# Kernel optimization log

Hardware: AMD Instinct MI355X
Metric: run time of the kernel (lower is better)

Reference implementation:

```python
import jax, jax.numpy as jnp
import numpy as np

B, T, E = 2048, 200, 64
H1, H2 = 64, 16
EPS = 1e-8


def dice(x, alpha):
    # Dice activation: standardize over (batch, seq) per feature, then
    # p = sigmoid(x_norm); out = p*x + (1-p)*alpha*x
    mean = jnp.mean(x, axis=(0, 1), keepdims=True)
    var = jnp.var(x, axis=(0, 1), keepdims=True)
    x_norm = (x - mean) * jax.lax.rsqrt(var + EPS)
    p = jax.nn.sigmoid(x_norm)
    return p * x + (1.0 - p) * alpha * x


def setup_inputs() -> dict:
    key = jax.random.key(0)
    ks = jax.random.split(key, 9)
    d_in = 4 * E
    return {
        "query_ad": jax.random.normal(ks[0], (B, 1, E), jnp.float32),
        "hist_behavior": jax.random.normal(ks[1], (B, T, E), jnp.float32),
        "hist_behavior_length": jax.random.randint(ks[2], (B,), 0, T, jnp.int64 if jax.config.jax_enable_x64 else jnp.int32),
        "W1": jax.random.normal(ks[3], (d_in, H1), jnp.float32) / np.sqrt(d_in),
        "b1": jnp.zeros((H1,), jnp.float32),
        "alpha1": jnp.zeros((H1,), jnp.float32),
        "W2": jax.random.normal(ks[4], (H1, H2), jnp.float32) / np.sqrt(H1),
        "b2": jnp.zeros((H2,), jnp.float32),
        "alpha2": jnp.zeros((H2,), jnp.float32),
    }


def reference(query_ad, hist_behavior, hist_behavior_length, W1, b1, alpha1, W2, b2, alpha2):
    Tlen = hist_behavior.shape[1]
    q = jnp.broadcast_to(query_ad, hist_behavior.shape)          # [B,T,E]
    att_in = jnp.concatenate(
        [q, hist_behavior, q - hist_behavior, q * hist_behavior], axis=-1
    )                                                            # [B,T,4E]
    h = dice(att_in @ W1 + b1, alpha1)                           # [B,T,H1]
    logits = dice(h @ W2 + b2, alpha2)                           # [B,T,H2]
    logits = jnp.swapaxes(logits, 1, 2)                          # [B,H2,T]
    mask = jnp.arange(Tlen)[None, :] < hist_behavior_length[:, None]  # [B,T]
    masked = jnp.where(mask[:, None, :], jnp.float32(1e-9), logits)
    score = jax.nn.softmax(masked, axis=-1)                      # [B,H2,T]
    out = jnp.einsum('bht,bte->bhe', score, hist_behavior)       # [B,H2,E]
    return out
```

## Files before the change

kernel.cpp:

```cpp
#include <hip/hip_runtime.h>
#include <math.h>


typedef float f4 __attribute__((ext_vector_type(4)));
typedef float f32x4 __attribute__((ext_vector_type(4)));
typedef short s8v __attribute__((ext_vector_type(8)));
typedef short s4v __attribute__((ext_vector_type(4)));
typedef unsigned short u16;

#define B_   2048
#define T_   200
#define BT_  409600
#define NB1  3200
#define NB2  1600

static __device__ __forceinline__ u16 f2bf(float f) {
  union { float f; unsigned u; } v; v.f = f;
  unsigned r = v.u + 0x7fffu + ((v.u >> 16) & 1u);
  return (u16)(r >> 16);
}
static __device__ __forceinline__ float bf2f(u16 s) {
  union { unsigned u; float f; } v; v.u = ((unsigned)s) << 16;
  return v.f;
}

__global__ __launch_bounds__(256) void k_qw(
    const float* __restrict__ q, const float* __restrict__ W1,
    const float* __restrict__ b1, float* __restrict__ qW) {
  __shared__ float Wac[64 * 65];
  __shared__ float ql[16 * 64];
  const int tid = threadIdx.x;
#pragma unroll
  for (int i = 0; i < 16; i++) {
    int idx = tid + 256 * i;
    int k = idx >> 6, j = idx & 63;
    Wac[k * 65 + j] = W1[k * 64 + j] + W1[(128 + k) * 64 + j];
  }
  const int b0 = blockIdx.x * 16;
#pragma unroll
  for (int i = 0; i < 4; i++) {
    int idx = tid + 256 * i;
    ql[idx] = q[(size_t)b0 * 64 + idx];
  }
  __syncthreads();
  const int wv = tid >> 6, lane = tid & 63;
#pragma unroll
  for (int ii = 0; ii < 4; ii++) {
    const int bl = wv * 4 + ii;
    float acc = b1[lane];
#pragma unroll 8
    for (int k = 0; k < 64; k++) acc += ql[bl * 64 + k] * Wac[k * 65 + lane];
    qW[(size_t)(b0 + bl) * 64 + lane] = acc;
  }
}

__global__ __launch_bounds__(256) void k_wprep(
    const float* __restrict__ W1, u16* __restrict__ wsWT) {
  int t = threadIdx.x + blockIdx.x * 256;
  int n = t >> 7, k = t & 127;
  float w = (k < 64) ? (W1[(64 + k) * 64 + n] - W1[(128 + k) * 64 + n])
                     : W1[(128 + k) * 64 + n];
  wsWT[t] = f2bf(w);
}

__global__ __launch_bounds__(256, 3) void k_gemm1(
    const float* __restrict__ q, const float* __restrict__ hist,
    const u16* __restrict__ wsWT, const float* __restrict__ qW,
    u16* __restrict__ z1, float* __restrict__ part1) {
  __shared__ __align__(16) u16 As[128 * 136];
  __shared__ __align__(16) u16 Ws[64 * 136];
  const int tid = threadIdx.x;
  const int R0 = blockIdx.x * 128;

#pragma unroll
  for (int i = 0; i < 4; i++) {
    int piece = tid + 256 * i;
    int n = piece >> 4, k8 = piece & 15;
    *(s8v*)(Ws + n * 136 + 8 * k8) = *(const s8v*)(wsWT + n * 128 + 8 * k8);
  }
#pragma unroll
  for (int i = 0; i < 8; i++) {
    int piece = tid + 256 * i;
    int row = piece >> 4, c4 = piece & 15;
    int R = R0 + row;
    int b = (int)((unsigned)R / 200u);
    f4 h4 = *(const f4*)(hist + (size_t)R * 64 + 4 * c4);
    f4 q4 = *(const f4*)(q + (size_t)b * 64 + 4 * c4);
    f4 p4 = h4 * q4;
    s4v hv, pv;
#pragma unroll
    for (int j = 0; j < 4; j++) { hv[j] = (short)f2bf(h4[j]); pv[j] = (short)f2bf(p4[j]); }
    *(s4v*)(As + row * 136 + 4 * c4) = hv;
    *(s4v*)(As + row * 136 + 64 + 4 * c4) = pv;
  }
  __syncthreads();

  const int wv = tid >> 6, lane = tid & 63;
  const int lm = lane & 15, quad = lane >> 4;
  f32x4 acc[2][4];
#pragma unroll
  for (int mt = 0; mt < 2; mt++)
#pragma unroll
    for (int nt = 0; nt < 4; nt++) acc[mt][nt] = (f32x4)0.f;

#pragma unroll
  for (int c = 0; c < 4; c++) {
    const int ko = 32 * c + 8 * quad;
    s8v a0 = *(const s8v*)(As + (32 * wv + lm) * 136 + ko);
    s8v a1 = *(const s8v*)(As + (32 * wv + 16 + lm) * 136 + ko);
#pragma unroll
    for (int nt = 0; nt < 4; nt++) {
      s8v b8 = *(const s8v*)(Ws + (16 * nt + lm) * 136 + ko);
      acc[0][nt] = __builtin_amdgcn_mfma_f32_16x16x32_bf16(a0, b8, acc[0][nt], 0, 0, 0);
      acc[1][nt] = __builtin_amdgcn_mfma_f32_16x16x32_bf16(a1, b8, acc[1][nt], 0, 0, 0);
    }
  }
  __syncthreads();

  u16* zs = As;
  float* red = (float*)Ws;
  const int g = wv * 4 + quad;
  float s[4] = {0.f, 0.f, 0.f, 0.f}, sq[4] = {0.f, 0.f, 0.f, 0.f};
#pragma unroll
  for (int mt = 0; mt < 2; mt++)
#pragma unroll
    for (int nt = 0; nt < 4; nt++)
#pragma unroll
      for (int r = 0; r < 4; r++) {
        int row = 32 * wv + 16 * mt + 4 * quad + r;
        int R = R0 + row;
        int b = (int)((unsigned)R / 200u);
        int col = 16 * nt + lm;
        float v = acc[mt][nt][r] + qW[(size_t)b * 64 + col];
        s[nt] += v; sq[nt] += v * v;
        zs[row * 72 + col] = f2bf(v);
      }
#pragma unroll
  for (int nt = 0; nt < 4; nt++) {
    red[g * 64 + 16 * nt + lm] = s[nt];
    red[1024 + g * 64 + 16 * nt + lm] = sq[nt];
  }
  __syncthreads();
#pragma unroll
  for (int i = 0; i < 4; i++) {
    int piece = tid + 256 * i;
    int row = piece >> 3, seg = piece & 7;
    s8v v = *(const s8v*)(zs + row * 72 + 8 * seg);
    *(s8v*)(z1 + (size_t)(R0 + row) * 64 + 8 * seg) = v;
  }
  if (tid < 64) {
    float ss = 0.f, qq = 0.f;
#pragma unroll
    for (int gg = 0; gg < 16; gg++) { ss += red[gg * 64 + tid]; qq += red[1024 + gg * 64 + tid]; }
    part1[(size_t)blockIdx.x * 128 + tid] = ss;
    part1[(size_t)blockIdx.x * 128 + 64 + tid] = qq;
  }
}

__global__ __launch_bounds__(256) void k_finalize(
    const float* __restrict__ part, float* __restrict__ statout,
    int nj, int stride, int nb, float invN) {
  const int j = blockIdx.x, tid = threadIdx.x;
  float s = 0.f, qq = 0.f;
  for (int i = tid; i < nb; i += 256) {
    s += part[(size_t)i * stride + j];
    qq += part[(size_t)i * stride + nj + j];
  }
#pragma unroll
  for (int off = 32; off > 0; off >>= 1) {
    s += __shfl_down(s, off);
    qq += __shfl_down(qq, off);
  }
  __shared__ float rs[4], rq[4];
  if ((tid & 63) == 0) { rs[tid >> 6] = s; rq[tid >> 6] = qq; }
  __syncthreads();
  if (tid == 0) {
    s = rs[0] + rs[1] + rs[2] + rs[3];
    qq = rq[0] + rq[1] + rq[2] + rq[3];
    float mean = s * invN;
    float var = qq * invN - mean * mean;
    statout[j] = mean;
    statout[nj + j] = rsqrtf(var + 1e-8f);
  }
}

__global__ __launch_bounds__(256) void k_gemm2(
    const u16* __restrict__ z1, const float* __restrict__ W2g,
    const float* __restrict__ b2, const float* __restrict__ alpha1,
    const float* __restrict__ stat1, float* __restrict__ z2,
    float* __restrict__ part2) {
  __shared__ float W2l[64 * 16];
  __shared__ float cf[208];
  __shared__ float red[256 * 33];
  const int tid = threadIdx.x;
  if (tid < 64) {
    cf[tid] = stat1[tid];
    cf[64 + tid] = stat1[64 + tid];
    cf[128 + tid] = alpha1[tid];
  }
  if (tid < 16) cf[192 + tid] = b2[tid];
#pragma unroll
  for (int i = 0; i < 4; i++) { int idx = tid + 256 * i; W2l[idx] = W2g[idx]; }
  __syncthreads();
  const size_t row = (size_t)blockIdx.x * 256 + tid;
  const u16* zr = z1 + row * 64;
  float acc[16];
#pragma unroll
  for (int j = 0; j < 16; j++) acc[j] = cf[192 + j];
  for (int k0 = 0; k0 < 64; k0 += 8) {
    s8v x8 = *(const s8v*)(zr + k0);
#pragma unroll
    for (int dk = 0; dk < 8; dk++) {
      int k = k0 + dk;
      float x = bf2f((u16)x8[dk]);
      float xn = (x - cf[k]) * cf[64 + k];
      float p = 1.f / (1.f + __expf(-xn));
      float h = x * (p + (1.f - p) * cf[128 + k]);
#pragma unroll
      for (int jc = 0; jc < 4; jc++) {
        f4 w = *(const f4*)(W2l + k * 16 + 4 * jc);
#pragma unroll
        for (int jj = 0; jj < 4; jj++) acc[4 * jc + jj] += h * w[jj];
      }
    }
  }
#pragma unroll
  for (int jc = 0; jc < 4; jc++) {
    f4 o;
#pragma unroll
    for (int jj = 0; jj < 4; jj++) o[jj] = acc[4 * jc + jj];
    *(f4*)(z2 + row * 16 + 4 * jc) = o;
  }
#pragma unroll
  for (int j = 0; j < 16; j++) {
    red[tid * 33 + j] = acc[j];
    red[tid * 33 + 16 + j] = acc[j] * acc[j];
  }
  __syncthreads();
  if (tid < 32) {
    float s = 0.f;
    for (int g = 0; g < 256; g++) s += red[g * 33 + tid];
    part2[(size_t)blockIdx.x * 32 + tid] = s;
  }
}

__global__ __launch_bounds__(256) void k_attn(
    const float* __restrict__ hist, const float* __restrict__ z2,
    const int* __restrict__ lens, const float* __restrict__ alpha2,
    const float* __restrict__ stat2, float* __restrict__ out) {
  __shared__ float lm[200 * 17];
  __shared__ float sc[16 * 200];
  const int tid = threadIdx.x;
  const int b = blockIdx.x;
  const int L = lens[b];
  {
    const int j = tid & 15, tb = tid >> 4;
    const float mu = stat2[j], rs = stat2[16 + j], al = alpha2[j];
    const float* z2b = z2 + (size_t)b * 3200;
#pragma unroll
    for (int i = 0; i < 13; i++) {
      int t = tb + 16 * i;
      if (t < 200) {
        float x = z2b[t * 16 + j];
        float xn = (x - mu) * rs;
        float p = 1.f / (1.f + __expf(-xn));
        float lg = x * (p + (1.f - p) * al);
        lm[t * 17 + j] = (t < L) ? 1e-9f : lg;
      }
    }
  }
  __syncthreads();
  {
    const int h = tid >> 4, s = tid & 15;
    float v[13];
    float m = -1e30f;
#pragma unroll
    for (int i = 0; i < 13; i++) {
      int t = s + 16 * i;
      float x = (t < 200) ? lm[t * 17 + h] : -1e30f;
      v[i] = x;
      m = fmaxf(m, x);
    }
#pragma unroll
    for (int mk = 8; mk > 0; mk >>= 1) m = fmaxf(m, __shfl_xor(m, mk, 16));
    float sum = 0.f;
#pragma unroll
    for (int i = 0; i < 13; i++) {
      int t = s + 16 * i;
      if (t < 200) { float e = __expf(v[i] - m); v[i] = e; sum += e; }
    }
#pragma unroll
    for (int mk = 8; mk > 0; mk >>= 1) sum += __shfl_xor(sum, mk, 16);
    const float inv = 1.f / sum;
#pragma unroll
    for (int i = 0; i < 13; i++) {
      int t = s + 16 * i;
      if (t < 200) sc[h * 200 + t] = v[i] * inv;
    }
  }
  __syncthreads();
  {
    const int h = tid >> 4, e0 = (tid & 15) * 4;
    const float* hb = hist + (size_t)b * 200 * 64 + e0;
    const float* sh = sc + h * 200;
    f4 acc = 0.f;
    for (int t = 0; t < 200; t += 4) {
      f4 h0 = *(const f4*)(hb + (size_t)t * 64);
      f4 h1 = *(const f4*)(hb + (size_t)(t + 1) * 64);
      f4 h2 = *(const f4*)(hb + (size_t)(t + 2) * 64);
      f4 h3 = *(const f4*)(hb + (size_t)(t + 3) * 64);
      acc += h0 * sh[t];
      acc += h1 * sh[t + 1];
      acc += h2 * sh[t + 2];
      acc += h3 * sh[t + 3];
    }
    *(f4*)(out + (size_t)b * 1024 + tid * 4) = acc;
  }
}

extern "C" void kernel_launch(void* const* d_in, const int* in_sizes, int n_in,
                              void* d_out, int out_size, void* d_ws, size_t ws_size,
                              hipStream_t stream) {
  const float* q    = (const float*)d_in[0];
  const float* hist = (const float*)d_in[1];
  const int*   len  = (const int*)d_in[2];
  const float* W1   = (const float*)d_in[3];
  const float* b1   = (const float*)d_in[4];
  const float* al1  = (const float*)d_in[5];
  const float* W2   = (const float*)d_in[6];
  const float* b2   = (const float*)d_in[7];
  const float* al2  = (const float*)d_in[8];
  float* out = (float*)d_out;

  char* ws = (char*)d_ws;
  u16*   z1    = (u16*)ws;
  float* z2    = (float*)(ws + 52428800);
  float* qW    = (float*)(ws + 52428800 + 26214400);
  u16*   wsWT  = (u16*)((char*)qW + 524288);
  float* part1 = (float*)((char*)wsWT + 16384);
  float* part2 = part1 + (size_t)NB1 * 128;
  float* stat1 = part2 + (size_t)NB2 * 32;
  float* stat2 = stat1 + 128;
  (void)ws_size; (void)in_sizes; (void)n_in; (void)out_size;

  k_qw<<<dim3(128), dim3(256), 0, stream>>>(q, W1, b1, qW);
  k_wprep<<<dim3(32), dim3(256), 0, stream>>>(W1, wsWT);
  k_gemm1<<<dim3(NB1), dim3(256), 0, stream>>>(q, hist, wsWT, qW, z1, part1);
  k_finalize<<<dim3(64), dim3(256), 0, stream>>>(part1, stat1, 64, 128, NB1, 1.f / (float)BT_);
  k_gemm2<<<dim3(NB2), dim3(256), 0, stream>>>(z1, W2, b2, al1, stat1, z2, part2);
  k_finalize<<<dim3(16), dim3(256), 0, stream>>>(part2, stat2, 16, 32, NB2, 1.f / (float)BT_);
  k_attn<<<dim3(B_), dim3(256), 0, stream>>>(hist, z2, len, al2, stat2, out);
}
```

Measured before the change: 282.7 us.

## Use MFMA for attention pooling, store z2 in bf16, fuse weight prep

Result: faster. 255.6 us (-9.6%).

```diff
diff --git a/kernel.cpp b/kernel.cpp
--- a/kernel.cpp
+++ b/kernel.cpp
@@ -26,7 +26,8 @@
 
 __global__ __launch_bounds__(256) void k_qw(
     const float* __restrict__ q, const float* __restrict__ W1,
-    const float* __restrict__ b1, float* __restrict__ qW) {
+    const float* __restrict__ b1, float* __restrict__ qW,
+    u16* __restrict__ wsWT) {
   __shared__ float Wac[64 * 65];
   __shared__ float ql[16 * 64];
   const int tid = threadIdx.x;
@@ -52,15 +53,13 @@
     for (int k = 0; k < 64; k++) acc += ql[bl * 64 + k] * Wac[k * 65 + lane];
     qW[(size_t)(b0 + bl) * 64 + lane] = acc;
   }
-}
-
-__global__ __launch_bounds__(256) void k_wprep(
-    const float* __restrict__ W1, u16* __restrict__ wsWT) {
-  int t = threadIdx.x + blockIdx.x * 256;
-  int n = t >> 7, k = t & 127;
-  float w = (k < 64) ? (W1[(64 + k) * 64 + n] - W1[(128 + k) * 64 + n])
-                     : W1[(128 + k) * 64 + n];
-  wsWT[t] = f2bf(w);
+  if (blockIdx.x < 32) {
+    int t = blockIdx.x * 256 + tid;
+    int n = t >> 7, k = t & 127;
+    float w = (k < 64) ? (W1[(64 + k) * 64 + n] - W1[(128 + k) * 64 + n])
+                       : W1[(128 + k) * 64 + n];
+    wsWT[t] = f2bf(w);
+  }
 }
 
 __global__ __launch_bounds__(256, 3) void k_gemm1(
@@ -96,7 +95,7 @@
   __syncthreads();
 
   const int wv = tid >> 6, lane = tid & 63;
-  const int lm = lane & 15, quad = lane >> 4;
+  const int lm16 = lane & 15, quad = lane >> 4;
   f32x4 acc[2][4];
 #pragma unroll
   for (int mt = 0; mt < 2; mt++)
@@ -106,11 +105,11 @@
 #pragma unroll
   for (int c = 0; c < 4; c++) {
     const int ko = 32 * c + 8 * quad;
-    s8v a0 = *(const s8v*)(As + (32 * wv + lm) * 136 + ko);
-    s8v a1 = *(const s8v*)(As + (32 * wv + 16 + lm) * 136 + ko);
+    s8v a0 = *(const s8v*)(As + (32 * wv + lm16) * 136 + ko);
+    s8v a1 = *(const s8v*)(As + (32 * wv + 16 + lm16) * 136 + ko);
 #pragma unroll
     for (int nt = 0; nt < 4; nt++) {
-      s8v b8 = *(const s8v*)(Ws + (16 * nt + lm) * 136 + ko);
+      s8v b8 = *(const s8v*)(Ws + (16 * nt + lm16) * 136 + ko);
       acc[0][nt] = __builtin_amdgcn_mfma_f32_16x16x32_bf16(a0, b8, acc[0][nt], 0, 0, 0);
       acc[1][nt] = __builtin_amdgcn_mfma_f32_16x16x32_bf16(a1, b8, acc[1][nt], 0, 0, 0);
     }
@@ -130,15 +129,15 @@
         int row = 32 * wv + 16 * mt + 4 * quad + r;
         int R = R0 + row;
         int b = (int)((unsigned)R / 200u);
-        int col = 16 * nt + lm;
+        int col = 16 * nt + lm16;
         float v = acc[mt][nt][r] + qW[(size_t)b * 64 + col];
         s[nt] += v; sq[nt] += v * v;
         zs[row * 72 + col] = f2bf(v);
       }
 #pragma unroll
   for (int nt = 0; nt < 4; nt++) {
-    red[g * 64 + 16 * nt + lm] = s[nt];
-    red[1024 + g * 64 + 16 * nt + lm] = sq[nt];
+    red[g * 64 + 16 * nt + lm16] = s[nt];
+    red[1024 + g * 64 + 16 * nt + lm16] = sq[nt];
   }
   __syncthreads();
 #pragma unroll
@@ -187,7 +186,7 @@
 __global__ __launch_bounds__(256) void k_gemm2(
     const u16* __restrict__ z1, const float* __restrict__ W2g,
     const float* __restrict__ b2, const float* __restrict__ alpha1,
-    const float* __restrict__ stat1, float* __restrict__ z2,
+    const float* __restrict__ stat1, u16* __restrict__ z2,
     float* __restrict__ part2) {
   __shared__ float W2l[64 * 16];
   __shared__ float cf[208];
@@ -224,49 +223,71 @@
       }
     }
   }
-#pragma unroll
-  for (int jc = 0; jc < 4; jc++) {
-    f4 o;
-#pragma unroll
-    for (int jj = 0; jj < 4; jj++) o[jj] = acc[4 * jc + jj];
-    *(f4*)(z2 + row * 16 + 4 * jc) = o;
-  }
+  s8v o0, o1;
+#pragma unroll
+  for (int jj = 0; jj < 8; jj++) { o0[jj] = (short)f2bf(acc[jj]); o1[jj] = (short)f2bf(acc[8 + jj]); }
+  *(s8v*)(z2 + row * 16) = o0;
+  *(s8v*)(z2 + row * 16 + 8) = o1;
 #pragma unroll
   for (int j = 0; j < 16; j++) {
     red[tid * 33 + j] = acc[j];
     red[tid * 33 + 16 + j] = acc[j] * acc[j];
   }
   __syncthreads();
-  if (tid < 32) {
-    float s = 0.f;
-    for (int g = 0; g < 256; g++) s += red[g * 33 + tid];
-    part2[(size_t)blockIdx.x * 32 + tid] = s;
-  }
-}
-
-__global__ __launch_bounds__(256) void k_attn(
-    const float* __restrict__ hist, const float* __restrict__ z2,
+  const int f = tid >> 3, sub = tid & 7;
+  float s = 0.f;
+  for (int g = sub; g < 256; g += 8) s += red[g * 33 + f];
+  s += __shfl_down(s, 4, 8);
+  s += __shfl_down(s, 2, 8);
+  s += __shfl_down(s, 1, 8);
+  if (sub == 0) part2[(size_t)blockIdx.x * 32 + f] = s;
+}
+
+__global__ __launch_bounds__(256, 3) void k_attn(
+    const float* __restrict__ hist, const u16* __restrict__ z2,
     const int* __restrict__ lens, const float* __restrict__ alpha2,
     const float* __restrict__ stat2, float* __restrict__ out) {
   __shared__ float lm[200 * 17];
-  __shared__ float sc[16 * 200];
+  __shared__ __align__(16) u16 scb[16 * 232];
+  __shared__ __align__(16) u16 hT[64 * 232];
+  __shared__ float cf2[48];
   const int tid = threadIdx.x;
   const int b = blockIdx.x;
   const int L = lens[b];
+  if (tid < 16) {
+    cf2[tid] = stat2[tid];
+    cf2[16 + tid] = stat2[16 + tid];
+    cf2[32 + tid] = alpha2[tid];
+  }
+  __syncthreads();
   {
-    const int j = tid & 15, tb = tid >> 4;
-    const float mu = stat2[j], rs = stat2[16 + j], al = alpha2[j];
-    const float* z2b = z2 + (size_t)b * 3200;
-#pragma unroll
-    for (int i = 0; i < 13; i++) {
-      int t = tb + 16 * i;
-      if (t < 200) {
-        float x = z2b[t * 16 + j];
-        float xn = (x - mu) * rs;
-        float p = 1.f / (1.f + __expf(-xn));
-        float lg = x * (p + (1.f - p) * al);
-        lm[t * 17 + j] = (t < L) ? 1e-9f : lg;
-      }
+    s8v zz = {0, 0, 0, 0, 0, 0, 0, 0};
+    for (int p = tid; p < 320; p += 256) {
+      if (p < 64) { int r = p >> 2, c = p & 3; *(s8v*)(scb + r * 232 + 200 + 8 * c) = zz; }
+      else { int pp = p - 64; int r = pp >> 2, c = pp & 3; *(s8v*)(hT + r * 232 + 200 + 8 * c) = zz; }
+    }
+  }
+  const float* hb = hist + (size_t)b * 200 * 64;
+#pragma unroll
+  for (int i = 0; i < 13; i++) {
+    int p = tid + 256 * i;
+    if (p < 3200) {
+      int t = p >> 4, eq = p & 15;
+      f4 h4 = *(const f4*)(hb + t * 64 + 4 * eq);
+#pragma unroll
+      for (int jj = 0; jj < 4; jj++) hT[(4 * eq + jj) * 232 + t] = f2bf(h4[jj]);
+    }
+  }
+  if (tid < 200) {
+    const u16* zr = z2 + ((size_t)b * 200 + tid) * 16;
+    s8v x0 = *(const s8v*)zr, x1 = *(const s8v*)(zr + 8);
+#pragma unroll
+    for (int j = 0; j < 16; j++) {
+      float x = bf2f((u16)(j < 8 ? x0[j] : x1[j - 8]));
+      float xn = (x - cf2[j]) * cf2[16 + j];
+      float p = 1.f / (1.f + __expf(-xn));
+      float lg = x * (p + (1.f - p) * cf2[32 + j]);
+      lm[tid * 17 + j] = (tid < L) ? 1e-9f : lg;
     }
   }
   __syncthreads();
@@ -295,26 +316,26 @@
 #pragma unroll
     for (int i = 0; i < 13; i++) {
       int t = s + 16 * i;
-      if (t < 200) sc[h * 200 + t] = v[i] * inv;
+      if (t < 200) scb[h * 232 + t] = f2bf(v[i] * inv);
     }
   }
   __syncthreads();
   {
-    const int h = tid >> 4, e0 = (tid & 15) * 4;
-    const float* hb = hist + (size_t)b * 200 * 64 + e0;
-    const float* sh = sc + h * 200;
-    f4 acc = 0.f;
-    for (int t = 0; t < 200; t += 4) {
-      f4 h0 = *(const f4*)(hb + (size_t)t * 64);
-      f4 h1 = *(const f4*)(hb + (size_t)(t + 1) * 64);
-      f4 h2 = *(const f4*)(hb + (size_t)(t + 2) * 64);
-      f4 h3 = *(const f4*)(hb + (size_t)(t + 3) * 64);
-      acc += h0 * sh[t];
-      acc += h1 * sh[t + 1];
-      acc += h2 * sh[t + 2];
-      acc += h3 * sh[t + 3];
-    }
-    *(f4*)(out + (size_t)b * 1024 + tid * 4) = acc;
+    const int wv = tid >> 6, lane = tid & 63;
+    const int lm16 = lane & 15, quad = lane >> 4;
+    f32x4 acc = {0.f, 0.f, 0.f, 0.f};
+#pragma unroll
+    for (int c = 0; c < 7; c++) {
+      const int ko = 32 * c + 8 * quad;
+      s8v a = *(const s8v*)(scb + lm16 * 232 + ko);
+      s8v bb = *(const s8v*)(hT + (16 * wv + lm16) * 232 + ko);
+      acc = __builtin_amdgcn_mfma_f32_16x16x32_bf16(a, bb, acc, 0, 0, 0);
+    }
+#pragma unroll
+    for (int r = 0; r < 4; r++) {
+      int h = 4 * quad + r;
+      out[(size_t)b * 1024 + h * 64 + 16 * wv + lm16] = acc[r];
+    }
   }
 }
 
@@ -334,8 +355,8 @@
 
   char* ws = (char*)d_ws;
   u16*   z1    = (u16*)ws;
-  float* z2    = (float*)(ws + 52428800);
-  float* qW    = (float*)(ws + 52428800 + 26214400);
+  u16*   z2    = (u16*)(ws + 52428800);
+  float* qW    = (float*)(ws + 52428800 + 13107200);
   u16*   wsWT  = (u16*)((char*)qW + 524288);
   float* part1 = (float*)((char*)wsWT + 16384);
   float* part2 = part1 + (size_t)NB1 * 128;
@@ -343,8 +364,7 @@
   float* stat2 = stat1 + 128;
   (void)ws_size; (void)in_sizes; (void)n_in; (void)out_size;
 
-  k_qw<<<dim3(128), dim3(256), 0, stream>>>(q, W1, b1, qW);
-  k_wprep<<<dim3(32), dim3(256), 0, stream>>>(W1, wsWT);
+  k_qw<<<dim3(128), dim3(256), 0, stream>>>(q, W1, b1, qW, wsWT);
   k_gemm1<<<dim3(NB1), dim3(256), 0, stream>>>(q, hist, wsWT, qW, z1, part1);
   k_finalize<<<dim3(64), dim3(256), 0, stream>>>(part1, stat1, 64, 128, NB1, 1.f / (float)BT_);
   k_gemm2<<<dim3(NB2), dim3(256), 0, stream>>>(z1, W2, b2, al1, stat1, z2, part2);
```
